# Performance work log

Hardware: AMD Instinct MI355X
Metric: run time of the kernel (lower is better)

The kernel has to match this reference:

```python
import jax, jax.numpy as jnp
import numpy as np

N_NODES = 100000
N_EDGES = 1600000
HIDDEN = 64
NUM_GRAPHS = 512


def setup_inputs() -> dict:
    key = jax.random.key(0)
    k1, k2, k3, k4, k5, k6 = jax.random.split(key, 6)
    x = jax.random.normal(k1, (N_NODES, HIDDEN), dtype=jnp.float32)
    edge_index = jax.random.randint(k2, (2, N_EDGES), 0, N_NODES, dtype=jnp.int64)
    batch = jnp.sort(jax.random.randint(k3, (N_NODES,), 0, NUM_GRAPHS, dtype=jnp.int64))
    # SAGPooling's internal GraphConv(64 -> 1): lin_rel (with bias) on aggregated
    # neighbor features, lin_root (no bias) on self features.
    s = 1.0 / np.sqrt(HIDDEN)
    W_rel = jax.random.uniform(k4, (HIDDEN, 1), dtype=jnp.float32, minval=-s, maxval=s)
    b_rel = jax.random.uniform(k5, (1,), dtype=jnp.float32, minval=-s, maxval=s)
    W_root = jax.random.uniform(k6, (HIDDEN, 1), dtype=jnp.float32, minval=-s, maxval=s)
    return {"x": x, "edge_index": edge_index, "batch": batch,
            "W_rel": W_rel, "b_rel": b_rel, "W_root": W_root}


def reference(x, edge_index, batch, W_rel, b_rel, W_root):
    n = x.shape[0]
    src, dst = edge_index[0], edge_index[1]
    # GraphConv (aggr='add'): sum x_j over in-edges, then lin_rel(aggr)+lin_root(x)
    aggr = jax.ops.segment_sum(x[src], dst, num_segments=n)          # [N, H]
    score = (aggr @ W_rel + b_rel + x @ W_root)[:, 0]                # [N]
    # min_score=-1 -> scores softmax-normalized per graph; all nodes kept in order
    m = jax.ops.segment_max(score, batch, num_segments=NUM_GRAPHS)   # [G]
    e = jnp.exp(score - m[batch])
    z = jax.ops.segment_sum(e, batch, num_segments=NUM_GRAPHS)       # [G]
    att = e / z[batch]                                               # [N]
    att_x = x * att[:, None]                                         # [N, H]
    # global_add_pool
    return jax.ops.segment_sum(att_x, batch, num_segments=NUM_GRAPHS)  # [G, H]
```

## Files before the change

kernel.cpp:

```cpp
#include <hip/hip_runtime.h>
#include <math.h>
#include <stdint.h>


#define H 64
#define TILE 4096
#define NTHR_S 512
#define EPT (TILE / NTHR_S)
#define BUCKET_SZ 256
#define MAX_NB 400
#define CAP 5120
#define ROWS_PER_WAVE 32
#define PSCALE 16384.0f
#define INV_PSCALE 6.103515625e-05f

__global__ __launch_bounds__(256) void node_prep(
    const float4* __restrict__ x4, const float* __restrict__ W_rel,
    const float* __restrict__ W_root,
    float* __restrict__ p, float* __restrict__ r,
    float* __restrict__ num, float* __restrict__ z,
    unsigned int* __restrict__ cursor,
    int n_nodes, int num_elems, int n_graphs, int nb)
{
    int gid = (int)(blockIdx.x * blockDim.x + threadIdx.x);
    if (gid < num_elems) num[gid] = 0.0f;
    else if (gid < num_elems + n_graphs) z[gid - num_elems] = 0.0f;
    else if (gid < num_elems + n_graphs + nb)
        cursor[gid - num_elems - n_graphs] =
            (unsigned int)(gid - num_elems - n_graphs) * CAP;

    int node = blockIdx.x * 64 + (threadIdx.x >> 2);
    int q    = threadIdx.x & 3;
    if (node >= n_nodes) return;

    float pv = 0.0f, rv = 0.0f;
    #pragma unroll
    for (int kk = 0; kk < 4; ++kk) {
        float4 v = x4[node * 16 + kk * 4 + q];
        int c0 = (kk * 4 + q) * 4;
        pv += v.x * W_rel[c0] + v.y * W_rel[c0 + 1]
            + v.z * W_rel[c0 + 2] + v.w * W_rel[c0 + 3];
        rv += v.x * W_root[c0] + v.y * W_root[c0 + 1]
            + v.z * W_root[c0 + 2] + v.w * W_root[c0 + 3];
    }
    pv += __shfl_xor(pv, 1, 64); pv += __shfl_xor(pv, 2, 64);
    rv += __shfl_xor(rv, 1, 64); rv += __shfl_xor(rv, 2, 64);
    if (q == 0) { p[node] = pv; r[node] = rv; }
}

__global__ __launch_bounds__(NTHR_S) void edge_sort(
    const int* __restrict__ src, const int* __restrict__ dst,
    const float* __restrict__ p,
    unsigned int* __restrict__ cursor, unsigned int* __restrict__ sorted_g,
    int n_edges, int nb)
{
    __shared__ unsigned int hist[MAX_NB];
    __shared__ unsigned int offs[MAX_NB];
    __shared__ unsigned int gbase[MAX_NB];
    __shared__ unsigned int tsum[NTHR_S];
    __shared__ unsigned int svals[TILE];
    __shared__ unsigned short sbid[TILE];

    int b = blockIdx.x;
    int base = b * TILE;
    int tile_n = min(TILE, n_edges - base);
    int tid = threadIdx.x;

    if (tid < nb) hist[tid] = 0;
    __syncthreads();

    unsigned int dd[EPT]; int ss[EPT];
    float pv[EPT];
    unsigned int bk[EPT], pk[EPT], slot[EPT];

    #pragma unroll
    for (int u = 0; u < EPT; ++u) {
        int j = tid + u * NTHR_S;
        if (j < tile_n) { dd[u] = (unsigned int)dst[base + j];
                          ss[u] = src[base + j]; }
        else dd[u] = 0xFFFFFFFFu;
    }
    #pragma unroll
    for (int u = 0; u < EPT; ++u)
        if (dd[u] != 0xFFFFFFFFu) pv[u] = p[ss[u]];
    #pragma unroll
    for (int u = 0; u < EPT; ++u) {
        if (dd[u] != 0xFFFFFFFFu) {
            bk[u] = dd[u] >> 8;
            int q = (int)__float2int_rn(pv[u] * PSCALE);
            q = max(-8388607, min(8388607, q));
            pk[u] = ((unsigned int)q << 8) | (dd[u] & 255u);
            slot[u] = atomicAdd(&hist[bk[u]], 1u);
        }
    }
    __syncthreads();

    unsigned int myv = (tid < nb) ? hist[tid] : 0;
    tsum[tid] = myv;
    __syncthreads();
    for (int d1 = 1; d1 < NTHR_S; d1 <<= 1) {
        unsigned int t2 = (tid >= d1) ? tsum[tid - d1] : 0;
        __syncthreads();
        tsum[tid] += t2;
        __syncthreads();
    }
    if (tid < nb) {
        offs[tid] = tsum[tid] - myv;
        gbase[tid] = myv ? atomicAdd(&cursor[tid], myv) : 0u;
    }
    __syncthreads();

    #pragma unroll
    for (int u = 0; u < EPT; ++u) {
        if (dd[u] != 0xFFFFFFFFu) {
            unsigned int pos = offs[bk[u]] + slot[u];
            svals[pos] = pk[u];
            sbid[pos]  = (unsigned short)bk[u];
        }
    }
    __syncthreads();

    for (int j = tid; j < tile_n; j += NTHR_S) {
        unsigned int bb = sbid[j];
        unsigned int gi = gbase[bb] + ((unsigned int)j - offs[bb]);
        if (gi < (bb + 1) * (unsigned int)CAP)
            sorted_g[gi] = svals[j];
    }
}

__global__ __launch_bounds__(256) void bucket_accum(
    const unsigned int* __restrict__ sorted_g,
    const unsigned int* __restrict__ cursor,
    const float* __restrict__ r,
    float* __restrict__ e_buf, int n_nodes)
{
    __shared__ int acc[BUCKET_SZ];
    int k = blockIdx.x;
    int tid = threadIdx.x;
    acc[tid] = 0;
    __syncthreads();

    unsigned int beg = (unsigned int)k * CAP;
    unsigned int cnt = min(cursor[k] - beg, (unsigned int)CAP);
    unsigned int n4  = cnt & ~3u;
    for (unsigned int j = tid * 4; j < n4; j += 1024) {
        uint4 v = *(const uint4*)(sorted_g + beg + j);
        atomicAdd(&acc[v.x & 255u], (int)v.x >> 8);
        atomicAdd(&acc[v.y & 255u], (int)v.y >> 8);
        atomicAdd(&acc[v.z & 255u], (int)v.z >> 8);
        atomicAdd(&acc[v.w & 255u], (int)v.w >> 8);
    }
    for (unsigned int j = n4 + tid; j < cnt; j += 256) {
        unsigned int v = sorted_g[beg + j];
        atomicAdd(&acc[v & 255u], (int)v >> 8);
    }
    __syncthreads();

    int node = k * BUCKET_SZ + tid;
    if (node < n_nodes)
        e_buf[node] = __expf((float)acc[tid] * INV_PSCALE + r[node]);
}

__global__ __launch_bounds__(256) void pool(
    const float* __restrict__ x, const float* __restrict__ e_buf,
    const int* __restrict__ batch,
    float* __restrict__ num, float* __restrict__ z, int n_nodes)
{
    int wid = threadIdx.x >> 6, lane = threadIdx.x & 63;
    int row0 = (blockIdx.x * 4 + wid) * ROWS_PER_WAVE;
    if (row0 >= n_nodes) return;
    int rend = min(row0 + ROWS_PER_WAVE, n_nodes);

    int g_first = batch[row0];
    int g_last  = batch[rend - 1];

    if (g_first == g_last && rend - row0 == ROWS_PER_WAVE) {
        float acc = 0.0f, acce = 0.0f;
        #pragma unroll 8
        for (int u = 0; u < ROWS_PER_WAVE; ++u) {
            int i = row0 + u;
            float e = e_buf[i];
            acc  += x[i * H + lane] * e;
            acce += e;
        }
        unsafeAtomicAdd(&num[g_first * H + lane], acc);
        if (lane == 0) unsafeAtomicAdd(&z[g_first], acce);
        return;
    }

    int cur_g = g_first;
    float acc = 0.0f, acce = 0.0f;
    for (int i = row0; i < rend; ++i) {
        int g = batch[i];
        if (g != cur_g) {
            unsafeAtomicAdd(&num[cur_g * H + lane], acc);
            if (lane == 0) unsafeAtomicAdd(&z[cur_g], acce);
            acc = 0.0f; acce = 0.0f;
            cur_g = g;
        }
        float e = e_buf[i];
        acc  += x[i * H + lane] * e;
        acce += e;
    }
    unsafeAtomicAdd(&num[cur_g * H + lane], acc);
    if (lane == 0) unsafeAtomicAdd(&z[cur_g], acce);
}

__global__ __launch_bounds__(256) void finalize(
    const float* __restrict__ num, const float* __restrict__ z,
    float* __restrict__ out, int num_elems)
{
    int i = (int)(blockIdx.x * blockDim.x + threadIdx.x);
    if (i >= num_elems) return;
    float zz = z[i >> 6];
    out[i] = (zz != 0.0f) ? num[i] / zz : 0.0f;
}

extern "C" void kernel_launch(void* const* d_in, const int* in_sizes, int n_in,
                              void* d_out, int out_size, void* d_ws, size_t ws_size,
                              hipStream_t stream)
{
    const float* x      = (const float*)d_in[0];
    const int*   eidx   = (const int*)d_in[1];
    const int*   batch  = (const int*)d_in[2];
    const float* W_rel  = (const float*)d_in[3];
    const float* W_root = (const float*)d_in[5];
    float* out = (float*)d_out;

    const int n_nodes  = in_sizes[0] / H;
    const int n_edges  = in_sizes[1] / 2;
    const int n_graphs = out_size / H;
    const int nb     = (n_nodes + BUCKET_SZ - 1) / BUCKET_SZ;
    const int ntiles = (n_edges + TILE - 1) / TILE;

    const int* src = eidx;
    const int* dst = eidx + n_edges;

    float* p     = (float*)d_ws;
    float* r     = p + n_nodes;
    float* e_buf = r + n_nodes;
    float* z     = e_buf + n_nodes;
    float* num   = z + n_graphs;
    unsigned int* cursor = (unsigned int*)(num + out_size);
    uintptr_t raw = (uintptr_t)(cursor + nb);
    unsigned int* sorted_g = (unsigned int*)((raw + 15) & ~(uintptr_t)15);

    int np_blocks = (n_nodes + 63) / 64;
    node_prep<<<np_blocks, 256, 0, stream>>>(
        (const float4*)x, W_rel, W_root, p, r, num, z, cursor,
        n_nodes, out_size, n_graphs, nb);
    edge_sort<<<ntiles, NTHR_S, 0, stream>>>(src, dst, p, cursor, sorted_g,
                                             n_edges, nb);
    bucket_accum<<<nb, 256, 0, stream>>>(sorted_g, cursor, r, e_buf, n_nodes);
    pool<<<(n_nodes + 4 * ROWS_PER_WAVE - 1) / (4 * ROWS_PER_WAVE), 256, 0, stream>>>(
        x, e_buf, batch, num, z, n_nodes);
    finalize<<<(out_size + 255) / 256, 256, 0, stream>>>(num, z, out, out_size);
}
```

Before: 126.6 us.

## Fuse bucket accumulation with pooling and use wave-shuffle scan in edge sort

Merges the bucket_accum and pool kernels into one 512-thread kernel per node bucket. Exp scores now stay in shared memory instead of going through a global e_buf, which removes one launch and a global round trip. Separately, edge_sort's block-wide Hillis-Steele scan over histogram bins is replaced by a single-wave shuffle scan with per-lane chunks, cutting many __syncthreads. In exchange, only 391 blocks run the fused pooling work, so parallelism for the x streaming drops compared with the separate pool launch.

After: 169.0 us. 33.5% more time.

```diff
diff --git a/kernel.cpp b/kernel.cpp
--- a/kernel.cpp
+++ b/kernel.cpp
@@ -10,7 +10,6 @@
 #define BUCKET_SZ 256
 #define MAX_NB 400
 #define CAP 5120
-#define ROWS_PER_WAVE 32
 #define PSCALE 16384.0f
 #define INV_PSCALE 6.103515625e-05f
 
@@ -57,7 +56,6 @@
     __shared__ unsigned int hist[MAX_NB];
     __shared__ unsigned int offs[MAX_NB];
     __shared__ unsigned int gbase[MAX_NB];
-    __shared__ unsigned int tsum[NTHR_S];
     __shared__ unsigned int svals[TILE];
     __shared__ unsigned short sbid[TILE];
 
@@ -95,18 +93,32 @@
     }
     __syncthreads();
 
-    unsigned int myv = (tid < nb) ? hist[tid] : 0;
-    tsum[tid] = myv;
-    __syncthreads();
-    for (int d1 = 1; d1 < NTHR_S; d1 <<= 1) {
-        unsigned int t2 = (tid >= d1) ? tsum[tid - d1] : 0;
-        __syncthreads();
-        tsum[tid] += t2;
-        __syncthreads();
-    }
-    if (tid < nb) {
-        offs[tid] = tsum[tid] - myv;
-        gbase[tid] = myv ? atomicAdd(&cursor[tid], myv) : 0u;
+    if (tid < 64) {
+        const int CH = (MAX_NB + 63) / 64;
+        unsigned int v[CH];
+        unsigned int tot = 0;
+        #pragma unroll
+        for (int c = 0; c < CH; ++c) {
+            int bin = tid * CH + c;
+            v[c] = (bin < nb) ? hist[bin] : 0;
+            tot += v[c];
+        }
+        unsigned int xs = tot;
+        #pragma unroll
+        for (int off = 1; off < 64; off <<= 1) {
+            unsigned int y = __shfl_up(xs, off, 64);
+            if (tid >= off) xs += y;
+        }
+        unsigned int run = xs - tot;
+        #pragma unroll
+        for (int c = 0; c < CH; ++c) {
+            int bin = tid * CH + c;
+            if (bin < nb) {
+                offs[bin] = run;
+                gbase[bin] = v[c] ? atomicAdd(&cursor[bin], v[c]) : 0u;
+                run += v[c];
+            }
+        }
     }
     __syncthreads();
 
@@ -128,82 +140,82 @@
     }
 }
 
-__global__ __launch_bounds__(256) void bucket_accum(
+__global__ __launch_bounds__(512) void bucket_pool(
     const unsigned int* __restrict__ sorted_g,
     const unsigned int* __restrict__ cursor,
-    const float* __restrict__ r,
-    float* __restrict__ e_buf, int n_nodes)
+    const float* __restrict__ r, const int* __restrict__ batch,
+    const float* __restrict__ x,
+    float* __restrict__ num, float* __restrict__ z, int n_nodes)
 {
     __shared__ int acc[BUCKET_SZ];
+    __shared__ float e_sh[BUCKET_SZ];
     int k = blockIdx.x;
     int tid = threadIdx.x;
-    acc[tid] = 0;
+    if (tid < BUCKET_SZ) acc[tid] = 0;
     __syncthreads();
 
     unsigned int beg = (unsigned int)k * CAP;
     unsigned int cnt = min(cursor[k] - beg, (unsigned int)CAP);
     unsigned int n4  = cnt & ~3u;
-    for (unsigned int j = tid * 4; j < n4; j += 1024) {
+    for (unsigned int j = tid * 4; j < n4; j += 2048) {
         uint4 v = *(const uint4*)(sorted_g + beg + j);
         atomicAdd(&acc[v.x & 255u], (int)v.x >> 8);
         atomicAdd(&acc[v.y & 255u], (int)v.y >> 8);
         atomicAdd(&acc[v.z & 255u], (int)v.z >> 8);
         atomicAdd(&acc[v.w & 255u], (int)v.w >> 8);
     }
-    for (unsigned int j = n4 + tid; j < cnt; j += 256) {
+    for (unsigned int j = n4 + tid; j < cnt; j += 512) {
         unsigned int v = sorted_g[beg + j];
         atomicAdd(&acc[v & 255u], (int)v >> 8);
     }
     __syncthreads();
 
-    int node = k * BUCKET_SZ + tid;
-    if (node < n_nodes)
-        e_buf[node] = __expf((float)acc[tid] * INV_PSCALE + r[node]);
-}
-
-__global__ __launch_bounds__(256) void pool(
-    const float* __restrict__ x, const float* __restrict__ e_buf,
-    const int* __restrict__ batch,
-    float* __restrict__ num, float* __restrict__ z, int n_nodes)
-{
-    int wid = threadIdx.x >> 6, lane = threadIdx.x & 63;
-    int row0 = (blockIdx.x * 4 + wid) * ROWS_PER_WAVE;
+    if (tid < BUCKET_SZ) {
+        int node = k * BUCKET_SZ + tid;
+        e_sh[tid] = (node < n_nodes)
+                  ? __expf((float)acc[tid] * INV_PSCALE + r[node]) : 0.0f;
+    }
+    __syncthreads();
+
+    int wid = tid >> 6, lane = tid & 63;
+    int row0 = k * BUCKET_SZ + wid * 32;
     if (row0 >= n_nodes) return;
-    int rend = min(row0 + ROWS_PER_WAVE, n_nodes);
+    int rend = min(row0 + 32, n_nodes);
+    int eoff = wid * 32;
 
     int g_first = batch[row0];
     int g_last  = batch[rend - 1];
 
-    if (g_first == g_last && rend - row0 == ROWS_PER_WAVE) {
-        float acc = 0.0f, acce = 0.0f;
+    if (g_first == g_last && rend - row0 == 32) {
+        float a = 0.0f, ae = 0.0f;
         #pragma unroll 8
-        for (int u = 0; u < ROWS_PER_WAVE; ++u) {
+        for (int u = 0; u < 32; ++u) {
             int i = row0 + u;
-            float e = e_buf[i];
-            acc  += x[i * H + lane] * e;
-            acce += e;
-        }
-        unsafeAtomicAdd(&num[g_first * H + lane], acc);
-        if (lane == 0) unsafeAtomicAdd(&z[g_first], acce);
+            float e = e_sh[eoff + u];
+            a  += x[i * H + lane] * e;
+            ae += e;
+        }
+        unsafeAtomicAdd(&num[g_first * H + lane], a);
+        if (lane == 0) unsafeAtomicAdd(&z[g_first], ae);
         return;
     }
 
     int cur_g = g_first;
-    float acc = 0.0f, acce = 0.0f;
+    float a = 0.0f, ae = 0.0f;
     for (int i = row0; i < rend; ++i) {
         int g = batch[i];
         if (g != cur_g) {
-            unsafeAtomicAdd(&num[cur_g * H + lane], acc);
-            if (lane == 0) unsafeAtomicAdd(&z[cur_g], acce);
-            acc = 0.0f; acce = 0.0f;
+            unsafeAtomicAdd(&num[cur_g * H + lane], a);
+            if (lane == 0) unsafeAtomicAdd(&z[cur_g], ae);
+            a = 0.0f; ae = 0.0f;
             cur_g = g;
         }
-        float e = e_buf[i];
-        acc  += x[i * H + lane] * e;
-        acce += e;
-    }
-    unsafeAtomicAdd(&num[cur_g * H + lane], acc);
-    if (lane == 0) unsafeAtomicAdd(&z[cur_g], acce);
+        float e = e_sh[i - k * BUCKET_SZ];
+        a  += x[i * H + lane] * e;
+        ae += e;
+    }
+    unsafeAtomicAdd(&num[cur_g * H + lane], a);
+    if (lane == 0) unsafeAtomicAdd(&z[cur_g], ae);
 }
 
 __global__ __launch_bounds__(256) void finalize(
@@ -236,11 +248,10 @@
     const int* src = eidx;
     const int* dst = eidx + n_edges;
 
-    float* p     = (float*)d_ws;
-    float* r     = p + n_nodes;
-    float* e_buf = r + n_nodes;
-    float* z     = e_buf + n_nodes;
-    float* num   = z + n_graphs;
+    float* p   = (float*)d_ws;
+    float* r   = p + n_nodes;
+    float* z   = r + n_nodes;
+    float* num = z + n_graphs;
     unsigned int* cursor = (unsigned int*)(num + out_size);
     uintptr_t raw = (uintptr_t)(cursor + nb);
     unsigned int* sorted_g = (unsigned int*)((raw + 15) & ~(uintptr_t)15);
@@ -251,8 +262,7 @@
         n_nodes, out_size, n_graphs, nb);
     edge_sort<<<ntiles, NTHR_S, 0, stream>>>(src, dst, p, cursor, sorted_g,
                                              n_edges, nb);
-    bucket_accum<<<nb, 256, 0, stream>>>(sorted_g, cursor, r, e_buf, n_nodes);
-    pool<<<(n_nodes + 4 * ROWS_PER_WAVE - 1) / (4 * ROWS_PER_WAVE), 256, 0, stream>>>(
-        x, e_buf, batch, num, z, n_nodes);
+    bucket_pool<<<nb, 512, 0, stream>>>(sorted_g, cursor, r, batch, x,
+                                        num, z, n_nodes);
     finalize<<<(out_size + 255) / 256, 256, 0, stream>>>(num, z, out, out_size);
 }
```
